# Performance work log

Measured on AMD Instinct MI355X. Metric: run time of the kernel, lower is better.

## Reference

```python
import jax, jax.numpy as jnp
import numpy as np

B = 65536
D_IN = 8
H1, H2 = 256, 256


def setup_inputs() -> dict:
    key = jax.random.key(0)
    ks = jax.random.split(key, 12)
    def lin(kw, kb, fan_in, fan_out):
        s = 1.0 / np.sqrt(fan_in)
        W = jax.random.uniform(kw, (fan_out, fan_in), jnp.float32, -s, s)
        b = jax.random.uniform(kb, (fan_out,), jnp.float32, -s, s)
        return W, b
    W0, b0 = lin(ks[0], ks[1], D_IN, H1)
    W1, b1 = lin(ks[2], ks[3], H1, H2)
    W2, b2 = lin(ks[4], ks[5], H2, 1)
    W3, b3 = lin(ks[6], ks[7], 1, 8)
    x_batch = jax.random.normal(ks[8], (B, D_IN), jnp.float32)
    scores_x_batch = jax.random.normal(ks[9], (B, D_IN), jnp.float32)
    c = jnp.zeros((), jnp.float32)  # init_val parameter
    return {"x_batch": x_batch, "scores_x_batch": scores_x_batch,
            "W0": W0, "b0": b0, "W1": W1, "b1": b1,
            "W2": W2, "b2": b2, "W3": W3, "b3": b3, "c": c}


def reference(x_batch, scores_x_batch, W0, b0, W1, b1, W2, b2, W3, b3, c):
    # singleforwardpass: tanh on all layers except the last
    def single(x):  # x: [8] -> [8]
        y = jnp.tanh(W0 @ x + b0)
        y = jnp.tanh(W1 @ y + b1)
        y = jnp.tanh(W2 @ y + b2)
        return W3 @ y + b3

    eye = jnp.eye(D_IN, dtype=x_batch.dtype)

    def per_sample(x, score):
        # jacobian(single, x).diag().sum() + dot(single(x), score) + c
        u, lin_fn = jax.linearize(single, x)
        J = jax.vmap(lin_fn)(eye)        # [8, 8] (columns of Jacobian as rows)
        div = jnp.trace(J)               # sum of Jacobian diagonal
        return c + div + jnp.dot(u, score)

    return jax.vmap(per_sample)(x_batch, scores_x_batch)  # [B]
```

## Files before the change

kernel.cpp:

```cpp
#include <hip/hip_runtime.h>
#include <hip/hip_bf16.h>

#define B_TOTAL 65536
#define H 256
#define TS 64
#define THREADS 512
#define STRIDE 264

typedef __attribute__((ext_vector_type(8))) short bf16x8;
typedef __attribute__((ext_vector_type(4))) float f32x4;

__device__ __forceinline__ void tanh_r(float x, float& t, float& r) {
    float e = __expf(x + x);
    r = __builtin_amdgcn_rcpf(e + 1.0f);
    t = fmaf(-2.0f, r, 1.0f);
}
__device__ __forceinline__ float bf2f(ushort b) {
    union { unsigned u; float f; } v; v.u = ((unsigned)b) << 16;
    return v.f;
}
__device__ __forceinline__ ushort f2bf(float f) {
    union { float f; unsigned u; } v; v.f = f;
    unsigned r = v.u + 0x7fffu + ((v.u >> 16) & 1u);
    return (ushort)(r >> 16);
}
__device__ __forceinline__ ushort2 cvt2(float a, float b) {
    union { __hip_bfloat162 h; ushort2 u; } v;
    v.h = __float22bfloat162_rn(make_float2(a, b));
    return v.u;
}
__device__ __forceinline__ bf16x8 pack8(float4 a, float4 b) {
    union { bf16x8 v; ushort2 u[4]; } r;
    r.u[0] = cvt2(a.x, a.y); r.u[1] = cvt2(a.z, a.w);
    r.u[2] = cvt2(b.x, b.y); r.u[3] = cvt2(b.z, b.w);
    return r.v;
}

__global__ void pack_weights(const float* __restrict__ W1, ushort* __restrict__ pack) {
    int g = blockIdx.x * 256 + threadIdx.x;
    int jt = g >> 9;
    int ks = (g >> 6) & 7;
    int l  = g & 63;
    int row = jt * 16 + (l & 15);
    int k0  = ks * 32 + (l >> 4) * 8;
    ushort* dst = pack + (size_t)g * 8;
    const float* src = W1 + (size_t)row * H + k0;
#pragma unroll
    for (int t = 0; t < 8; ++t) dst[t] = f2bf(src[t]);
}

__launch_bounds__(THREADS, 4)
__global__ void fused_mlp(const float* __restrict__ x_batch,
                          const float* __restrict__ scores,
                          const float* __restrict__ W0, const float* __restrict__ b0,
                          const float* __restrict__ b1,
                          const float* __restrict__ W2, const float* __restrict__ b2,
                          const float* __restrict__ W3, const float* __restrict__ b3,
                          const float* __restrict__ cptr,
                          const ushort* __restrict__ packs,
                          float* __restrict__ out) {
    __shared__ ushort Y0[TS][STRIDE];
    __shared__ ushort DG[TS][STRIDE];
    __shared__ float  G0[H];
    __shared__ float  Z2p[8][TS];
    __shared__ float  Trp[8][TS];

    const int tid  = threadIdx.x;
    const int lane = tid & 63;
    const int w    = tid >> 6;
    const int bs   = blockIdx.x * TS;
    const int cl   = lane & 15;
    const int q    = lane >> 4;
    const int rq   = q * 4;
    const int j0   = w * 32;

    bf16x8 wfrag[16];
    {
        const ushort* pW = packs + (size_t)(2 * w) * 4096 + (size_t)lane * 8;
#pragma unroll
        for (int ks = 0; ks < 8; ++ks) {
            wfrag[ks * 2 + 0] = *(const bf16x8*)(pW + ks * 512);
            wfrag[ks * 2 + 1] = *(const bf16x8*)(pW + 4096 + ks * 512);
        }
    }

    if (tid < H) {
        const float* wr = W0 + (size_t)tid * 8;
        float4 wa = *(const float4*)wr, wb = *(const float4*)(wr + 4);
        float4 w3a = *(const float4*)W3, w3b = *(const float4*)(W3 + 4);
        G0[tid] = wa.x * w3a.x + wa.y * w3a.y + wa.z * w3a.z + wa.w * w3a.w
                + wb.x * w3b.x + wb.y * w3b.y + wb.z * w3b.z + wb.w * w3b.w;
    }

    f32x4 l0[2][4];
    {
        bf16x8 bx[4];
#pragma unroll
        for (int st = 0; st < 4; ++st) {
            bf16x8 p = (bf16x8){0, 0, 0, 0, 0, 0, 0, 0};
            if (q == 0) {
                const float* xr = x_batch + (size_t)(bs + st * 16 + cl) * 8;
                p = pack8(*(const float4*)xr, *(const float4*)(xr + 4));
            }
            bx[st] = p;
        }
        const float* wr0 = W0 + (size_t)(j0 + cl) * 8;
        const float* wr1 = W0 + (size_t)(j0 + 16 + cl) * 8;
        bf16x8 af0 = pack8(*(const float4*)wr0, *(const float4*)(wr0 + 4));
        bf16x8 af1 = pack8(*(const float4*)wr1, *(const float4*)(wr1 + 4));
#pragma unroll
        for (int st = 0; st < 4; ++st) {
            f32x4 z = (f32x4){0.f, 0.f, 0.f, 0.f};
            l0[0][st] = __builtin_amdgcn_mfma_f32_16x16x32_bf16(af0, bx[st], z, 0, 0, 0);
            l0[1][st] = __builtin_amdgcn_mfma_f32_16x16x32_bf16(af1, bx[st], z, 0, 0, 0);
        }
    }
    __syncthreads();

    {
        float4 b0v0 = *(const float4*)(b0 + j0 + rq);
        float4 b0v1 = *(const float4*)(b0 + j0 + 16 + rq);
        float4 g0v0 = *(const float4*)&G0[j0 + rq];
        float4 g0v1 = *(const float4*)&G0[j0 + 16 + rq];
#pragma unroll
        for (int st = 0; st < 4; ++st) {
            const int row = st * 16 + cl;
#pragma unroll
            for (int jt = 0; jt < 2; ++jt) {
                f32x4 z = l0[jt][st];
                float4 bv = jt ? b0v1 : b0v0;
                float4 gv = jt ? g0v1 : g0v0;
                float t0, t1, t2, t3, r0, r1, r2, r3;
                tanh_r(z[0] + bv.x, t0, r0); tanh_r(z[1] + bv.y, t1, r1);
                tanh_r(z[2] + bv.z, t2, r2); tanh_r(z[3] + bv.w, t3, r3);
                ushort2 lo = cvt2(t0, t1), hi = cvt2(t2, t3);
                ushort4 vv; vv.x = lo.x; vv.y = lo.y; vv.z = hi.x; vv.w = hi.y;
                *(ushort4*)&Y0[row][j0 + jt * 16 + rq] = vv;
                float m0 = 4.f * r0, m1 = 4.f * r1, m2 = 4.f * r2, m3 = 4.f * r3;
                float d0 = fmaf(-m0, r0, m0), d1 = fmaf(-m1, r1, m1);
                float d2 = fmaf(-m2, r2, m2), d3 = fmaf(-m3, r3, m3);
                lo = cvt2(d0 * gv.x, d1 * gv.y); hi = cvt2(d2 * gv.z, d3 * gv.w);
                vv.x = lo.x; vv.y = lo.y; vv.z = hi.x; vv.w = hi.y;
                *(ushort4*)&DG[row][j0 + jt * 16 + rq] = vv;
            }
        }
    }
    __syncthreads();

    ushort4 aph[2][4];
    {
        f32x4 facc[2][4];
#pragma unroll
        for (int jt = 0; jt < 2; ++jt)
#pragma unroll
            for (int st = 0; st < 4; ++st) facc[jt][st] = (f32x4){0.f, 0.f, 0.f, 0.f};
#pragma unroll
        for (int ks = 0; ks < 8; ++ks) {
            const int k0 = ks * 32 + q * 8;
            bf16x8 by[4];
#pragma unroll
            for (int st = 0; st < 4; ++st)
                by[st] = *(const bf16x8*)&Y0[st * 16 + cl][k0];
#pragma unroll
            for (int st = 0; st < 4; ++st) {
                facc[0][st] = __builtin_amdgcn_mfma_f32_16x16x32_bf16(wfrag[ks * 2 + 0], by[st], facc[0][st], 0, 0, 0);
                facc[1][st] = __builtin_amdgcn_mfma_f32_16x16x32_bf16(wfrag[ks * 2 + 1], by[st], facc[1][st], 0, 0, 0);
            }
        }
        float4 b1v0 = *(const float4*)(b1 + j0 + rq);
        float4 b1v1 = *(const float4*)(b1 + j0 + 16 + rq);
        float4 w2v0 = *(const float4*)(W2 + j0 + rq);
        float4 w2v1 = *(const float4*)(W2 + j0 + 16 + rq);
#pragma unroll
        for (int st = 0; st < 4; ++st) {
            float zp = 0.f;
#pragma unroll
            for (int jt = 0; jt < 2; ++jt) {
                f32x4 z = facc[jt][st];
                float4 bv = jt ? b1v1 : b1v0;
                float4 wv = jt ? w2v1 : w2v0;
                float t0, t1, t2, t3, r0, r1, r2, r3;
                tanh_r(z[0] + bv.x, t0, r0); tanh_r(z[1] + bv.y, t1, r1);
                tanh_r(z[2] + bv.z, t2, r2); tanh_r(z[3] + bv.w, t3, r3);
                zp = fmaf(wv.x, t0, zp); zp = fmaf(wv.y, t1, zp);
                zp = fmaf(wv.z, t2, zp); zp = fmaf(wv.w, t3, zp);
                float m0 = 4.f * wv.x * r0, m1 = 4.f * wv.y * r1;
                float m2 = 4.f * wv.z * r2, m3 = 4.f * wv.w * r3;
                ushort2 lo = cvt2(fmaf(-m0, r0, m0), fmaf(-m1, r1, m1));
                ushort2 hi = cvt2(fmaf(-m2, r2, m2), fmaf(-m3, r3, m3));
                ushort4 av; av.x = lo.x; av.y = lo.y; av.z = hi.x; av.w = hi.y;
                aph[jt][st] = av;
            }
            zp += __shfl_xor(zp, 16);
            zp += __shfl_xor(zp, 32);
            if (lane < 16) Z2p[w][st * 16 + lane] = zp;
        }
    }
    __syncthreads();

#pragma unroll
    for (int st = 0; st < 4; ++st)
#pragma unroll
        for (int jt = 0; jt < 2; ++jt)
            *(ushort4*)&Y0[st * 16 + cl][j0 + jt * 16 + rq] = aph[jt][st];

    {
        f32x4 bacc[2][4];
#pragma unroll
        for (int jt = 0; jt < 2; ++jt)
#pragma unroll
            for (int st = 0; st < 4; ++st) bacc[jt][st] = (f32x4){0.f, 0.f, 0.f, 0.f};
#pragma unroll
        for (int ks = 0; ks < 8; ++ks) {
            const int k0 = ks * 32 + q * 8;
            bf16x8 bd[4];
#pragma unroll
            for (int st = 0; st < 4; ++st)
                bd[st] = *(const bf16x8*)&DG[st * 16 + cl][k0];
#pragma unroll
            for (int st = 0; st < 4; ++st) {
                bacc[0][st] = __builtin_amdgcn_mfma_f32_16x16x32_bf16(wfrag[ks * 2 + 0], bd[st], bacc[0][st], 0, 0, 0);
                bacc[1][st] = __builtin_amdgcn_mfma_f32_16x16x32_bf16(wfrag[ks * 2 + 1], bd[st], bacc[1][st], 0, 0, 0);
            }
        }
#pragma unroll
        for (int st = 0; st < 4; ++st) {
            float tp = 0.f;
#pragma unroll
            for (int jt = 0; jt < 2; ++jt) {
                ushort4 a4 = *(const ushort4*)&Y0[st * 16 + cl][j0 + jt * 16 + rq];
                f32x4 m = bacc[jt][st];
                tp = fmaf(bf2f(a4.x), m[0], tp);
                tp = fmaf(bf2f(a4.y), m[1], tp);
                tp = fmaf(bf2f(a4.z), m[2], tp);
                tp = fmaf(bf2f(a4.w), m[3], tp);
            }
            tp += __shfl_xor(tp, 16);
            tp += __shfl_xor(tp, 32);
            if (lane < 16) Trp[w][st * 16 + lane] = tp;
        }
    }
    __syncthreads();

    if (tid < TS) {
        const int s = tid;
        float z2 = b2[0], tr = 0.f;
#pragma unroll
        for (int k = 0; k < 8; ++k) { z2 += Z2p[k][s]; tr += Trp[k][s]; }
        float y2, r2;
        tanh_r(z2, y2, r2);
        float m2 = 4.0f * r2;
        float dy2 = fmaf(-m2, r2, m2);
        float4 w3a = *(const float4*)W3;
        float4 w3b = *(const float4*)(W3 + 4);
        float4 b3a = *(const float4*)b3;
        float4 b3b = *(const float4*)(b3 + 4);
        const float* sc = scores + (size_t)(bs + s) * 8;
        float4 s0 = *(const float4*)sc;
        float4 s1 = *(const float4*)(sc + 4);
        float p1 = w3a.x * s0.x + w3a.y * s0.y + w3a.z * s0.z + w3a.w * s0.w
                 + w3b.x * s1.x + w3b.y * s1.y + w3b.z * s1.z + w3b.w * s1.w;
        float p2 = b3a.x * s0.x + b3a.y * s0.y + b3a.z * s0.z + b3a.w * s0.w
                 + b3b.x * s1.x + b3b.y * s1.y + b3b.z * s1.z + b3b.w * s1.w;
        out[bs + s] = cptr[0] + dy2 * tr + fmaf(y2, p1, p2);
    }
}

extern "C" void kernel_launch(void* const* d_in, const int* in_sizes, int n_in,
                              void* d_out, int out_size, void* d_ws, size_t ws_size,
                              hipStream_t stream) {
    const float* x  = (const float*)d_in[0];
    const float* sc = (const float*)d_in[1];
    const float* W0 = (const float*)d_in[2];
    const float* b0 = (const float*)d_in[3];
    const float* W1 = (const float*)d_in[4];
    const float* b1 = (const float*)d_in[5];
    const float* W2 = (const float*)d_in[6];
    const float* b2 = (const float*)d_in[7];
    const float* W3 = (const float*)d_in[8];
    const float* b3 = (const float*)d_in[9];
    const float* c  = (const float*)d_in[10];
    float* out = (float*)d_out;
    ushort* packs = (ushort*)d_ws;

    hipLaunchKernelGGL(pack_weights, dim3(32), dim3(256), 0, stream, W1, packs);
    hipLaunchKernelGGL(fused_mlp, dim3(B_TOTAL / TS), dim3(THREADS), 0, stream,
                       x, sc, W0, b0, b1, W2, b2, W3, b3, c, packs, out);
}
```

Before: 37.26 us.

## Fuse forward and tangent layer-1 MFMA loops, stream weight fragments from global

```diff
diff --git a/kernel.cpp b/kernel.cpp
--- a/kernel.cpp
+++ b/kernel.cpp
@@ -74,15 +74,9 @@
     const int rq   = q * 4;
     const int j0   = w * 32;
 
-    bf16x8 wfrag[16];
-    {
-        const ushort* pW = packs + (size_t)(2 * w) * 4096 + (size_t)lane * 8;
-#pragma unroll
-        for (int ks = 0; ks < 8; ++ks) {
-            wfrag[ks * 2 + 0] = *(const bf16x8*)(pW + ks * 512);
-            wfrag[ks * 2 + 1] = *(const bf16x8*)(pW + 4096 + ks * 512);
-        }
-    }
+    const ushort* pW = packs + (size_t)(2 * w) * 4096 + (size_t)lane * 8;
+    bf16x8 wf0 = *(const bf16x8*)(pW);
+    bf16x8 wf1 = *(const bf16x8*)(pW + 4096);
 
     if (tid < H) {
         const float* wr = W0 + (size_t)tid * 8;
@@ -147,36 +141,46 @@
     }
     __syncthreads();
 
-    ushort4 aph[2][4];
+    f32x4 facc[2][4], bacc[2][4];
+#pragma unroll
+    for (int jt = 0; jt < 2; ++jt)
+#pragma unroll
+        for (int st = 0; st < 4; ++st) {
+            facc[jt][st] = (f32x4){0.f, 0.f, 0.f, 0.f};
+            bacc[jt][st] = (f32x4){0.f, 0.f, 0.f, 0.f};
+        }
+#pragma unroll
+    for (int ks = 0; ks < 8; ++ks) {
+        bf16x8 nf0 = wf0, nf1 = wf1;
+        if (ks < 7) {
+            nf0 = *(const bf16x8*)(pW + (size_t)(ks + 1) * 512);
+            nf1 = *(const bf16x8*)(pW + 4096 + (size_t)(ks + 1) * 512);
+        }
+        const int k0 = ks * 32 + q * 8;
+#pragma unroll
+        for (int st = 0; st < 4; ++st) {
+            bf16x8 by = *(const bf16x8*)&Y0[st * 16 + cl][k0];
+            bf16x8 bd = *(const bf16x8*)&DG[st * 16 + cl][k0];
+            facc[0][st] = __builtin_amdgcn_mfma_f32_16x16x32_bf16(wf0, by, facc[0][st], 0, 0, 0);
+            facc[1][st] = __builtin_amdgcn_mfma_f32_16x16x32_bf16(wf1, by, facc[1][st], 0, 0, 0);
+            bacc[0][st] = __builtin_amdgcn_mfma_f32_16x16x32_bf16(wf0, bd, bacc[0][st], 0, 0, 0);
+            bacc[1][st] = __builtin_amdgcn_mfma_f32_16x16x32_bf16(wf1, bd, bacc[1][st], 0, 0, 0);
+        }
+        wf0 = nf0; wf1 = nf1;
+    }
+
     {
-        f32x4 facc[2][4];
-#pragma unroll
-        for (int jt = 0; jt < 2; ++jt)
-#pragma unroll
-            for (int st = 0; st < 4; ++st) facc[jt][st] = (f32x4){0.f, 0.f, 0.f, 0.f};
-#pragma unroll
-        for (int ks = 0; ks < 8; ++ks) {
-            const int k0 = ks * 32 + q * 8;
-            bf16x8 by[4];
-#pragma unroll
-            for (int st = 0; st < 4; ++st)
-                by[st] = *(const bf16x8*)&Y0[st * 16 + cl][k0];
-#pragma unroll
-            for (int st = 0; st < 4; ++st) {
-                facc[0][st] = __builtin_amdgcn_mfma_f32_16x16x32_bf16(wfrag[ks * 2 + 0], by[st], facc[0][st], 0, 0, 0);
-                facc[1][st] = __builtin_amdgcn_mfma_f32_16x16x32_bf16(wfrag[ks * 2 + 1], by[st], facc[1][st], 0, 0, 0);
-            }
-        }
         float4 b1v0 = *(const float4*)(b1 + j0 + rq);
         float4 b1v1 = *(const float4*)(b1 + j0 + 16 + rq);
         float4 w2v0 = *(const float4*)(W2 + j0 + rq);
         float4 w2v1 = *(const float4*)(W2 + j0 + 16 + rq);
 #pragma unroll
         for (int st = 0; st < 4; ++st) {
-            float zp = 0.f;
+            float zp = 0.f, tp = 0.f;
 #pragma unroll
             for (int jt = 0; jt < 2; ++jt) {
-                f32x4 z = facc[jt][st];
+                f32x4 z  = facc[jt][st];
+                f32x4 mm = bacc[jt][st];
                 float4 bv = jt ? b1v1 : b1v0;
                 float4 wv = jt ? w2v1 : w2v0;
                 float t0, t1, t2, t3, r0, r1, r2, r3;
@@ -186,58 +190,19 @@
                 zp = fmaf(wv.z, t2, zp); zp = fmaf(wv.w, t3, zp);
                 float m0 = 4.f * wv.x * r0, m1 = 4.f * wv.y * r1;
                 float m2 = 4.f * wv.z * r2, m3 = 4.f * wv.w * r3;
-                ushort2 lo = cvt2(fmaf(-m0, r0, m0), fmaf(-m1, r1, m1));
-                ushort2 hi = cvt2(fmaf(-m2, r2, m2), fmaf(-m3, r3, m3));
-                ushort4 av; av.x = lo.x; av.y = lo.y; av.z = hi.x; av.w = hi.y;
-                aph[jt][st] = av;
+                float a0 = fmaf(-m0, r0, m0), a1 = fmaf(-m1, r1, m1);
+                float a2 = fmaf(-m2, r2, m2), a3 = fmaf(-m3, r3, m3);
+                tp = fmaf(a0, mm[0], tp); tp = fmaf(a1, mm[1], tp);
+                tp = fmaf(a2, mm[2], tp); tp = fmaf(a3, mm[3], tp);
             }
             zp += __shfl_xor(zp, 16);
             zp += __shfl_xor(zp, 32);
-            if (lane < 16) Z2p[w][st * 16 + lane] = zp;
-        }
-    }
-    __syncthreads();
-
-#pragma unroll
-    for (int st = 0; st < 4; ++st)
-#pragma unroll
-        for (int jt = 0; jt < 2; ++jt)
-            *(ushort4*)&Y0[st * 16 + cl][j0 + jt * 16 + rq] = aph[jt][st];
-
-    {
-        f32x4 bacc[2][4];
-#pragma unroll
-        for (int jt = 0; jt < 2; ++jt)
-#pragma unroll
-            for (int st = 0; st < 4; ++st) bacc[jt][st] = (f32x4){0.f, 0.f, 0.f, 0.f};
-#pragma unroll
-        for (int ks = 0; ks < 8; ++ks) {
-            const int k0 = ks * 32 + q * 8;
-            bf16x8 bd[4];
-#pragma unroll
-            for (int st = 0; st < 4; ++st)
-                bd[st] = *(const bf16x8*)&DG[st * 16 + cl][k0];
-#pragma unroll
-            for (int st = 0; st < 4; ++st) {
-                bacc[0][st] = __builtin_amdgcn_mfma_f32_16x16x32_bf16(wfrag[ks * 2 + 0], bd[st], bacc[0][st], 0, 0, 0);
-                bacc[1][st] = __builtin_amdgcn_mfma_f32_16x16x32_bf16(wfrag[ks * 2 + 1], bd[st], bacc[1][st], 0, 0, 0);
-            }
-        }
-#pragma unroll
-        for (int st = 0; st < 4; ++st) {
-            float tp = 0.f;
-#pragma unroll
-            for (int jt = 0; jt < 2; ++jt) {
-                ushort4 a4 = *(const ushort4*)&Y0[st * 16 + cl][j0 + jt * 16 + rq];
-                f32x4 m = bacc[jt][st];
-                tp = fmaf(bf2f(a4.x), m[0], tp);
-                tp = fmaf(bf2f(a4.y), m[1], tp);
-                tp = fmaf(bf2f(a4.z), m[2], tp);
-                tp = fmaf(bf2f(a4.w), m[3], tp);
-            }
             tp += __shfl_xor(tp, 16);
             tp += __shfl_xor(tp, 32);
-            if (lane < 16) Trp[w][st * 16 + lane] = tp;
+            if (lane < 16) {
+                Z2p[w][st * 16 + lane] = zp;
+                Trp[w][st * 16 + lane] = tp;
+            }
         }
     }
     __syncthreads();
```

New measurement: 34.62 us. -7.1%, faster.
